# Kernel tuning notes

Measured on AMD Instinct MI355X. Metric: run time of the kernel, lower is better.

## Reference

```python
import jax, jax.numpy as jnp
import numpy as np

B, T, V, H, L = 32, 128, 50257, 1024, 2


def setup_inputs() -> dict:
    key = jax.random.key(0)
    ks = jax.random.split(key, 8)
    s_in = 0.02   # small init to keep gates unsaturated
    return {
        "tokens": jax.random.randint(ks[0], (B, T), 0, V, dtype=jnp.int32),
        "embedding": jax.random.normal(ks[1], (V, H), jnp.float32) * s_in,
        "W_ih": jax.random.normal(ks[2], (L, 4 * H, H), jnp.float32) * s_in,
        "W_hh": jax.random.normal(ks[3], (L, 4 * H, H), jnp.float32) * s_in,
        "b_ih": jax.random.normal(ks[4], (L, 4 * H), jnp.float32) * s_in,
        "b_hh": jax.random.normal(ks[5], (L, 4 * H), jnp.float32) * s_in,
        "W_out": jax.random.normal(ks[6], (V, H), jnp.float32) * s_in,
        "b_out": jax.random.normal(ks[7], (V,), jnp.float32) * s_in,
        "h0": jnp.zeros((L, B, H), jnp.float32),
        "c0": jnp.zeros((L, B, H), jnp.float32),
    }


def reference(tokens, embedding, W_ih, W_hh, b_ih, b_hh, W_out, b_out, h0, c0):
    # Teacher-forced LSTM LM: embed -> L-layer LSTM (PyTorch gate order i,f,g,o)
    # -> vocab projection -> log-softmax. Dropout is identity (p=0 / eval).
    x = embedding[tokens]                      # [B,T,H]
    xs = jnp.swapaxes(x, 0, 1)                 # [T,B,H] time-major for scan
    n_layers = W_ih.shape[0]

    def step(carry, x_t):
        h, c = carry                           # each [L,B,H]
        inp = x_t
        hs, cs = [], []
        for l in range(n_layers):
            gates = inp @ W_ih[l].T + b_ih[l] + h[l] @ W_hh[l].T + b_hh[l]  # [B,4H]
            i_g, f_g, g_g, o_g = jnp.split(gates, 4, axis=-1)
            i_g = jax.nn.sigmoid(i_g)
            f_g = jax.nn.sigmoid(f_g)
            g_g = jnp.tanh(g_g)
            o_g = jax.nn.sigmoid(o_g)
            c_new = f_g * c[l] + i_g * g_g
            h_new = o_g * jnp.tanh(c_new)
            hs.append(h_new)
            cs.append(c_new)
            inp = h_new
        return (jnp.stack(hs), jnp.stack(cs)), inp

    (hT, cT), outs = jax.lax.scan(step, (h0, c0), xs)   # outs: [T,B,H]
    outs = jnp.swapaxes(outs, 0, 1)                     # [B,T,H]
    logits = outs @ W_out.T + b_out                     # [B,T,V]
    logp = jax.nn.log_softmax(logits, axis=-1)
    return logp, hT, cT
```

## Files before the change

### kernel.cpp

```cpp
#include <hip/hip_runtime.h>
#include <hip/hip_bf16.h>
#include <cstdint>
#include <cstddef>

#define DEVI __device__ __forceinline__

typedef __attribute__((ext_vector_type(8))) short short8;
typedef __attribute__((ext_vector_type(4))) float f32x4;
using u16 = unsigned short;

constexpr int BSZ = 32, TSZ = 128, VSZ = 50257, HSZ = 1024;
constexpr int M4 = BSZ * TSZ;
constexpr int FH = 4 * HSZ;
constexpr long long OUT_LOGP = (long long)M4 * VSZ;
constexpr int NWRK = 192;
constexpr int NBLK = 256;
constexpr int LDSB = 147584;
constexpr int LDBF = 50258;
constexpr int NNT = 393;
constexpr int CVT_PER = 20;
constexpr int CVTILES = 64 * CVT_PER;

DEVI u16 f2bf(float f) {
  unsigned u = __float_as_uint(f);
  unsigned r = (u + 0x7fffu + ((u >> 16) & 1u)) >> 16;
  return (u16)r;
}
DEVI u16 f2bf_hw(float f) {
  __hip_bfloat16 h = __float2bfloat16(f);
  return __builtin_bit_cast(u16, h);
}
DEVI float bf2f(u16 u) { return __uint_as_float(((unsigned)u) << 16); }
DEVI float sigm(float x) { return 1.f / (1.f + __expf(-x)); }
DEVI float tanh_fast(float x) { return 1.f - 2.f / (1.f + __expf(2.f * x)); }

DEVI f32x4 mfma16(short8 a, short8 b, f32x4 c) {
  return __builtin_amdgcn_mfma_f32_16x16x32_bf16(a, b, c, 0, 0, 0);
}

DEVI void gld16(const void* g, void* l) {
  auto gp = (const __attribute__((address_space(1))) unsigned int*)g;
  auto lp = (__attribute__((address_space(3))) unsigned int*)l;
  __builtin_amdgcn_global_load_lds(gp, lp, 16, 0, 0);
}

DEVI void cohld16x16(const u16* base, short8 (&d)[16]) {
  asm volatile(
      "global_load_dwordx4 %0, %16, off sc0 sc1\n\t"
      "global_load_dwordx4 %1, %16, off offset:64 sc0 sc1\n\t"
      "global_load_dwordx4 %2, %16, off offset:128 sc0 sc1\n\t"
      "global_load_dwordx4 %3, %16, off offset:192 sc0 sc1\n\t"
      "global_load_dwordx4 %4, %16, off offset:256 sc0 sc1\n\t"
      "global_load_dwordx4 %5, %16, off offset:320 sc0 sc1\n\t"
      "global_load_dwordx4 %6, %16, off offset:384 sc0 sc1\n\t"
      "global_load_dwordx4 %7, %16, off offset:448 sc0 sc1\n\t"
      "global_load_dwordx4 %8, %16, off offset:512 sc0 sc1\n\t"
      "global_load_dwordx4 %9, %16, off offset:576 sc0 sc1\n\t"
      "global_load_dwordx4 %10, %16, off offset:640 sc0 sc1\n\t"
      "global_load_dwordx4 %11, %16, off offset:704 sc0 sc1\n\t"
      "global_load_dwordx4 %12, %16, off offset:768 sc0 sc1\n\t"
      "global_load_dwordx4 %13, %16, off offset:832 sc0 sc1\n\t"
      "global_load_dwordx4 %14, %16, off offset:896 sc0 sc1\n\t"
      "global_load_dwordx4 %15, %16, off offset:960 sc0 sc1\n\t"
      "s_waitcnt vmcnt(0)"
      : "=&v"(d[0]), "=&v"(d[1]), "=&v"(d[2]), "=&v"(d[3]),
        "=&v"(d[4]), "=&v"(d[5]), "=&v"(d[6]), "=&v"(d[7]),
        "=&v"(d[8]), "=&v"(d[9]), "=&v"(d[10]), "=&v"(d[11]),
        "=&v"(d[12]), "=&v"(d[13]), "=&v"(d[14]), "=&v"(d[15])
      : "v"(base)
      : "memory");
}
DEVI void cohst2_u16(u16* p0, u16 v0, u16* p1, u16 v1) {
  asm volatile(
      "global_store_short %0, %2, off sc0 sc1\n\t"
      "global_store_short %1, %3, off sc0 sc1\n\t"
      "s_waitcnt vmcnt(0)"
      :: "v"(p0), "v"(p1), "v"((unsigned)v0), "v"((unsigned)v1)
      : "memory");
}
DEVI void cohst1_u16(u16* p0, u16 v0) {
  asm volatile(
      "global_store_short %0, %1, off sc0 sc1\n\t"
      "s_waitcnt vmcnt(0)"
      :: "v"(p0), "v"((unsigned)v0)
      : "memory");
}
DEVI void flagst(unsigned* p, unsigned v) {
  __hip_atomic_store(p, v, __ATOMIC_RELAXED, __HIP_MEMORY_SCOPE_AGENT);
}
DEVI unsigned flagld(const unsigned* p) {
  return __hip_atomic_load(p, __ATOMIC_RELAXED, __HIP_MEMORY_SCOPE_AGENT);
}

DEVI void wait64(const unsigned* f, unsigned g, int l) {
  while (!__all((int)(flagld(f + l) >= g))) __builtin_amdgcn_s_sleep(1);
}
DEVI void wait128(const unsigned* f, unsigned g, int l) {
  for (;;) {
    unsigned a = flagld(f + l);
    unsigned b = flagld(f + 64 + l);
    if (__all((int)((a >= g) && (b >= g)))) break;
    __builtin_amdgcn_s_sleep(1);
  }
}

__global__ void prep_all(const float* __restrict__ bih, const float* __restrict__ bhh,
                         float* __restrict__ bias0, float* __restrict__ rowsum,
                         unsigned* __restrict__ bar, const float* __restrict__ h0,
                         u16* __restrict__ H0, u16* __restrict__ h1init) {
  int i = blockIdx.x * 256 + threadIdx.x;
  H0[i] = f2bf(h0[i]);
  h1init[i] = f2bf(h0[BSZ * HSZ + i]);
  if (i < FH) { bias0[i] = bih[i] + bhh[i]; rowsum[i] = 0.f; }
  if (i < 1024) bar[i] = 0u;
}

__global__ void cvt_bf16(const float* __restrict__ src, u16* __restrict__ dst, int n4) {
  int i = blockIdx.x * blockDim.x + threadIdx.x;
  int stride = gridDim.x * blockDim.x;
  for (; i < n4; i += stride) {
    float4 v = ((const float4*)src)[i];
    ushort4 o; o.x = f2bf(v.x); o.y = f2bf(v.y); o.z = f2bf(v.z); o.w = f2bf(v.w);
    ((ushort4*)dst)[i] = o;
  }
}

__global__ __launch_bounds__(256) void embed_kernel(const int* __restrict__ tok,
                                                    const float* __restrict__ emb,
                                                    u16* __restrict__ X) {
  int m = blockIdx.x;
  int t = m >> 5, b = m & 31;
  int token = tok[b * TSZ + t];
  const float4* src = (const float4*)(emb + (size_t)token * HSZ);
  int i = threadIdx.x;
  float4 v = src[i];
  ushort4 o; o.x = f2bf(v.x); o.y = f2bf(v.y); o.z = f2bf(v.z); o.w = f2bf(v.w);
  *(ushort4*)(X + (size_t)m * HSZ + i * 4) = o;
}

template <int EPI, bool BCVT, bool TMAJ>
DEVI void gemm_tile(char* smemg, const u16* __restrict__ A, const void* __restrict__ Bsrc,
                    void* __restrict__ Cout, const float* __restrict__ bias,
                    float* __restrict__ rowsum, int m0, int n0, int N, int K, int ldc) {
  u16* As = (u16*)smemg;
  u16* Bs = (u16*)(smemg + 8192);
  float* epi = (float*)smemg;
  const int tid = threadIdx.x;
  const int l = tid & 63, wid = tid >> 6;
  const int wm = wid >> 1, wn = wid & 1;

  const int srow = tid >> 2, sq = tid & 3;
  const int arow0 = m0 + srow, arow1 = m0 + 64 + srow;
  int brow0 = n0 + srow;      if (brow0 > N - 1) brow0 = N - 1;
  int brow1 = n0 + 64 + srow; if (brow1 > N - 1) brow1 = N - 1;

  const u16* Bbf = (const u16*)Bsrc;
  const float* Bf32 = (const float*)Bsrc;
  u16* AsW = As + (size_t)(tid >> 6) * 512;
  u16* BsW = Bs + (size_t)(tid >> 6) * 512;

  f32x4 acc[4][4];
  f32x4 z = {0.f, 0.f, 0.f, 0.f};
#pragma unroll
  for (int a = 0; a < 4; ++a)
#pragma unroll
    for (int b = 0; b < 4; ++b) acc[a][b] = z;

  for (int k0 = 0; k0 < K; k0 += 32) {
    gld16(A + (size_t)arow0 * K + k0 + sq * 8, AsW);
    gld16(A + (size_t)arow1 * K + k0 + sq * 8, AsW + 2048);
    if (!BCVT) {
      gld16(Bbf + (size_t)brow0 * K + k0 + sq * 8, BsW);
      gld16(Bbf + (size_t)brow1 * K + k0 + sq * 8, BsW + 2048);
    } else {
      const float* s0 = Bf32 + (size_t)brow0 * K + k0 + sq * 8;
      const float* s1 = Bf32 + (size_t)brow1 * K + k0 + sq * 8;
      float4 x0 = *(const float4*)s0, y0 = *(const float4*)(s0 + 4);
      float4 x1 = *(const float4*)s1, y1 = *(const float4*)(s1 + 4);
      short8 v0, v1;
      v0[0]=(short)f2bf(x0.x); v0[1]=(short)f2bf(x0.y); v0[2]=(short)f2bf(x0.z); v0[3]=(short)f2bf(x0.w);
      v0[4]=(short)f2bf(y0.x); v0[5]=(short)f2bf(y0.y); v0[6]=(short)f2bf(y0.z); v0[7]=(short)f2bf(y0.w);
      v1[0]=(short)f2bf(x1.x); v1[1]=(short)f2bf(x1.y); v1[2]=(short)f2bf(x1.z); v1[3]=(short)f2bf(x1.w);
      v1[4]=(short)f2bf(y1.x); v1[5]=(short)f2bf(y1.y); v1[6]=(short)f2bf(y1.z); v1[7]=(short)f2bf(y1.w);
      *(short8*)&Bs[(size_t)tid * 8] = v0;
      *(short8*)&Bs[(size_t)tid * 8 + 2048] = v1;
    }
    __syncthreads();
    short8 af[4], bfr[4];
#pragma unroll
    for (int x = 0; x < 4; ++x) {
      int ar = wm * 64 + x * 16 + (l & 15);
      af[x] = *(const short8*)&As[ar * 32 + ((l >> 4) << 3)];
      int br = wn * 64 + x * 16 + (l & 15);
      bfr[x] = *(const short8*)&Bs[br * 32 + ((l >> 4) << 3)];
    }
#pragma unroll
    for (int mf = 0; mf < 4; ++mf)
#pragma unroll
      for (int nf = 0; nf < 4; ++nf)
        acc[mf][nf] = mfma16(af[mf], bfr[nf], acc[mf][nf]);
    __syncthreads();
  }

  if constexpr (EPI == 2) {
    u16* C = (u16*)Cout;
#pragma unroll
    for (int mf = 0; mf < 4; ++mf) {
      int rbase = m0 + wm * 64 + mf * 16 + ((l >> 4) << 2);
      float bvr[4];
#pragma unroll
      for (int j = 0; j < 4; ++j) bvr[j] = bias[rbase + j];
#pragma unroll
      for (int nf = 0; nf < 4; ++nf) {
        int cg = n0 + wn * 64 + nf * 16 + (l & 15);
#pragma unroll
        for (int j = 0; j < 4; ++j)
          C[(size_t)(rbase + j) * ldc + cg] = f2bf_hw(acc[mf][nf][j] + bvr[j]);
      }
    }
  } else if constexpr (EPI == 3) {
    u16* C = (u16*)Cout;
    float* ep = epi + wid * 1024;
    const int lq4 = l >> 4, l15e = l & 15;
    float bv[4];
#pragma unroll
    for (int nf = 0; nf < 4; ++nf) {
      int cg = n0 + wn * 64 + nf * 16 + l15e;
      bv[nf] = (cg < N) ? bias[cg] : 0.f;
    }
    const int r8 = l >> 3, c8 = l & 7;
    const int colb8 = n0 + wn * 64 + c8 * 8;
#pragma unroll
    for (int mf = 0; mf < 4; ++mf) {
#pragma unroll
      for (int nf = 0; nf < 4; ++nf)
#pragma unroll
        for (int j = 0; j < 4; ++j)
          ep[(lq4 * 4 + j) * 64 + nf * 16 + l15e] = acc[mf][nf][j] + bv[nf];
      asm volatile("s_waitcnt lgkmcnt(0)" ::: "memory");
      __builtin_amdgcn_sched_barrier(0);
#pragma unroll
      for (int pass = 0; pass < 2; ++pass) {
        const int rr = pass * 8 + r8;
        f32x4 v0 = *(const f32x4*)&ep[rr * 64 + c8 * 8];
        f32x4 v1 = *(const f32x4*)&ep[rr * 64 + c8 * 8 + 4];
        const int row = m0 + wm * 64 + mf * 16 + rr;
        const int orow = TMAJ ? ((row & 31) * TSZ + (row >> 5)) : row;
        float e = 0.f;
        if (colb8 + 7 < N) {
          short8 o;
          o[0]=(short)f2bf_hw(v0[0]); o[1]=(short)f2bf_hw(v0[1]);
          o[2]=(short)f2bf_hw(v0[2]); o[3]=(short)f2bf_hw(v0[3]);
          o[4]=(short)f2bf_hw(v1[0]); o[5]=(short)f2bf_hw(v1[1]);
          o[6]=(short)f2bf_hw(v1[2]); o[7]=(short)f2bf_hw(v1[3]);
          *(short8*)&C[(size_t)orow * ldc + colb8] = o;
          e = __expf(v0[0]) + __expf(v0[1]) + __expf(v0[2]) + __expf(v0[3]) +
              __expf(v1[0]) + __expf(v1[1]) + __expf(v1[2]) + __expf(v1[3]);
        } else {
#pragma unroll
          for (int kk = 0; kk < 8; ++kk) {
            float fv = (kk < 4) ? v0[kk] : v1[kk - 4];
            if (colb8 + kk < N) {
              C[(size_t)orow * ldc + colb8 + kk] = f2bf_hw(fv);
              e += __expf(fv);
            }
          }
        }
        e += __shfl_xor(e, 1, 8); e += __shfl_xor(e, 2, 8); e += __shfl_xor(e, 4, 8);
        if (c8 == 0) atomicAdd(&rowsum[orow], e);
      }
      asm volatile("s_waitcnt lgkmcnt(0)" ::: "memory");
      __builtin_amdgcn_sched_barrier(0);
    }
  } else {
    float* C = (float*)Cout;
    float* ep = epi + wid * 1024;
    const int lq4 = l >> 4, l15e = l & 15;
    float bv[4];
#pragma unroll
    for (int nf = 0; nf < 4; ++nf) {
      int cg = n0 + wn * 64 + nf * 16 + l15e;
      bv[nf] = (cg < N) ? bias[cg] : 0.f;
    }
    const int colbase = n0 + wn * 64 + l15e * 4;
#pragma unroll
    for (int mf = 0; mf < 4; ++mf) {
#pragma unroll
      for (int nf = 0; nf < 4; ++nf)
#pragma unroll
        for (int j = 0; j < 4; ++j)
          ep[(lq4 * 4 + j) * 64 + nf * 16 + l15e] = acc[mf][nf][j] + bv[nf];
      asm volatile("s_waitcnt lgkmcnt(0)" ::: "memory");
      __builtin_amdgcn_sched_barrier(0);
#pragma unroll
      for (int pass = 0; pass < 4; ++pass) {
        const int rr = pass * 4 + lq4;
        f32x4 v = *(const f32x4*)&ep[rr * 64 + l15e * 4];
        const int row = m0 + wm * 64 + mf * 16 + rr;
        const int orow = TMAJ ? ((row & 31) * TSZ + (row >> 5)) : row;
        float e = 0.f;
        if (colbase + 3 < N) {
          *(f32x4*)&C[(size_t)orow * ldc + colbase] = v;
          e = __expf(v[0]) + __expf(v[1]) + __expf(v[2]) + __expf(v[3]);
        } else {
#pragma unroll
          for (int kk = 0; kk < 4; ++kk)
            if (colbase + kk < N) {
              C[(size_t)orow * ldc + colbase + kk] = v[kk];
              e += __expf(v[kk]);
            }
        }
        e += __shfl_xor(e, 1, 16); e += __shfl_xor(e, 2, 16);
        e += __shfl_xor(e, 4, 16); e += __shfl_xor(e, 8, 16);
        if (l15e == 0) atomicAdd(&rowsum[orow], e);
      }
      asm volatile("s_waitcnt lgkmcnt(0)" ::: "memory");
      __builtin_amdgcn_sched_barrier(0);
    }
  }
}

template <int EPI, bool BCVT, int MAP, bool TMAJ>
__global__ __launch_bounds__(256) void gemm_bt(const u16* __restrict__ A,
                                               const void* __restrict__ Bsrc,
                                               void* __restrict__ Cout,
                                               const float* __restrict__ bias,
                                               float* __restrict__ rowsum,
                                               int nm, int nn, int N, int K, int ldc,
                                               int wofs) {
  __shared__ char smemg[16384];
  const int id = blockIdx.x;
  int bm, bn;
  if constexpr (MAP == 2) {
    const int gsz = (int)gridDim.x;
    int wg = ((gsz & 7) == 0) ? (id % 8) * (gsz >> 3) + (id >> 3) : id;
    int w = wofs + wg;
    bm = w / nn; bn = w % nn;
  } else {
    const int gsz = nm * nn;
    int wg = ((gsz & 7) == 0) ? (id % 8) * (gsz >> 3) + (id >> 3) : id;
    bm = wg % nm; bn = wg / nm;
  }
  gemm_tile<EPI, BCVT, TMAJ>(smemg, A, Bsrc, Cout, bias, rowsum,
                             bm * 128, bn * 128, N, K, ldc);
}

struct LstmArgs {
  const u16* G0T;
  const float* Wih;
  const float* Whh;
  const float* bih, *bhh, *c0;
  u16* H0;
  u16* H1;
  const u16* h1init;
  float* out_hc;
  unsigned* bar;
  const float* Wout;
  u16* Woutbf;
  u16* Lbf;
  const float* bout;
  float* rowsum;
  int mode;
};

DEVI void stage_row_q(const float* src, char* row, int sw, int q) {
  for (int kk = 0; kk < 256; kk += 8) {
    float4 x = *(const float4*)(src + kk);
    float4 y = *(const float4*)(src + kk + 4);
    short8 v;
    v[0]=(short)f2bf(x.x); v[1]=(short)f2bf(x.y); v[2]=(short)f2bf(x.z); v[3]=(short)f2bf(x.w);
    v[4]=(short)f2bf(y.x); v[5]=(short)f2bf(y.y); v[6]=(short)f2bf(y.z); v[7]=(short)f2bf(y.w);
    const int kbyte = (q * 256 + kk) * 2;
    *(short8*)(row + (kbyte ^ sw)) = v;
  }
}

DEVI short8 ldsB(const char* lds, int r, int kbyte) {
  return *(const short8*)(lds + (size_t)r * 2048 + (kbyte ^ ((r & 7) << 4)));
}

DEVI void part_wr(float* part, int wstride_log2, int wv, int R, int lq, f32x4 v) {
  *(f32x4*)&part[(wv << wstride_log2) + (R << 4) + ((lq ^ (R & 3)) << 2)] = v;
}
DEVI float part_rd(const float* part, int wstride_log2, int wv, int R, int c) {
  return part[(wv << wstride_log2) + (R << 4) + ((((c >> 2) ^ (R & 3)) << 2)) + (c & 3)];
}

__global__ __launch_bounds__(256, 1) void lstm_coop(LstmArgs A) {
  extern __shared__ char smem[];
  const int wg = blockIdx.x, tid = threadIdx.x;
  const int wv = tid >> 6, l = tid & 63;
  const int l15 = l & 15, lq = l >> 4;
  const int bh = wv >> 1, kh = wv & 1;

  if (wg < 64) {
    char* WL = smem;
    float* part = (float*)(smem + 131072);
    const int j0 = wg << 4;
    {
      const int R = tid >> 2, q = tid & 3;
      const int grow = ((R >> 4) << 10) + j0 + (R & 15);
      stage_row_q(A.Whh + (size_t)grow * HSZ + q * 256, WL + (size_t)R * 2048,
                  (R & 7) << 4, q);
    }
    const int uu = tid & 15, bb = tid >> 4;
    float cst[2];
    cst[0] = A.c0[(size_t)bb * HSZ + j0 + uu];
    cst[1] = A.c0[(size_t)(bb + 16) * HSZ + j0 + uu];
    __syncthreads();
    unsigned* myflag = A.bar + wg;

    for (int t = 0; t < TSZ; ++t) {
      float g0v[4][2];
      {
        const int col = t * 32;
#pragma unroll
        for (int g4 = 0; g4 < 4; ++g4) {
          const u16* gp = A.G0T + (size_t)((g4 << 10) + j0 + uu) * M4 + col;
          g0v[g4][0] = bf2f(gp[bb]);
          g0v[g4][1] = bf2f(gp[bb + 16]);
        }
      }
      if (t > 0) wait64(A.bar, (unsigned)t, l);
      const u16* hprev = A.H0 + (size_t)t * (BSZ * HSZ);
      const u16* hb = hprev + (size_t)(bh * 16 + l15) * HSZ + (kh << 9) + (lq << 3);
      short8 a[16];
      cohld16x16(hb, a);
      __builtin_amdgcn_sched_barrier(0);
      f32x4 acc[4];
      { f32x4 z = {0.f,0.f,0.f,0.f}; acc[0]=z; acc[1]=z; acc[2]=z; acc[3]=z; }
#pragma unroll
      for (int k = 0; k < 16; ++k) {
        const int kbyte = (((kh << 4) + k) << 6) + (lq << 4);
#pragma unroll
        for (int tr = 0; tr < 4; ++tr)
          acc[tr] = mfma16(a[k], ldsB(WL, (tr << 4) + l15, kbyte), acc[tr]);
      }
#pragma unroll
      for (int tr = 0; tr < 4; ++tr)
        part_wr(part, 10, wv, (tr << 4) + l15, lq, acc[tr]);
      __syncthreads();
      const bool last = (t == TSZ - 1);
      u16* hnext = A.H0 + (size_t)(t + 1) * (BSZ * HSZ);
      u16 hv[2];
#pragma unroll
      for (int pp = 0; pp < 2; ++pp) {
        const int b = bb + (pp << 4);
        float gi = g0v[0][pp], gf = g0v[1][pp], gg = g0v[2][pp], go = g0v[3][pp];
#pragma unroll
        for (int kh2 = 0; kh2 < 2; ++kh2) {
          const int w2 = (pp << 1) | kh2;
          gi += part_rd(part, 10, w2, uu, bb);
          gf += part_rd(part, 10, w2, 16 + uu, bb);
          gg += part_rd(part, 10, w2, 32 + uu, bb);
          go += part_rd(part, 10, w2, 48 + uu, bb);
        }
        float i_ = sigm(gi), f_ = sigm(gf), g_ = tanh_fast(gg), o_ = sigm(go);
        float c_ = f_ * cst[pp] + i_ * g_;
        cst[pp] = c_;
        float h_ = o_ * tanh_fast(c_);
        hv[pp] = f2bf(h_);
        if (last) {
          A.out_hc[(size_t)b * HSZ + j0 + uu] = h_;
          A.out_hc[2 * BSZ * HSZ + (size_t)b * HSZ + j0 + uu] = c_;
        }
      }
      cohst2_u16(hnext + (size_t)bb * HSZ + j0 + uu, hv[0],
                 hnext + (size_t)(bb + 16) * HSZ + j0 + uu, hv[1]);
      __syncthreads();
      if (tid == 0) flagst(myflag, (unsigned)(t + 1));
    }
  } else if (wg < NWRK) {
    char* WxL = smem;
    char* WhL = smem + 65536;
    float* part = (float*)(smem + 131072);
    float* biasL = (float*)(smem + 139264);
    const int lw = wg - 64;
    const int j1 = lw << 3;
    {
      const int rr = tid >> 2, q = tid & 3;
      const int r = rr & 31;
      const int grow = FH + ((r >> 3) << 10) + j1 + (r & 7);
      const float* base = (rr >= 32) ? A.Whh : A.Wih;
      char* dst = ((rr >= 32) ? WhL : WxL) + (size_t)r * 2048;
      stage_row_q(base + (size_t)grow * HSZ + q * 256, dst, (r & 7) << 4, q);
    }
    if (tid < 32) {
      const int grow = FH + ((tid >> 3) << 10) + j1 + (tid & 7);
      biasL[tid] = A.bih[grow] + A.bhh[grow];
    }
    const int uu = tid & 7, b1 = tid >> 3;
    float cst = A.c0[BSZ * HSZ + (size_t)b1 * HSZ + j1 + uu];
    __syncthreads();
    unsigned* myflag = A.bar + 64 + lw;

    for (int t = 0; t < TSZ; ++t) {
      wait64(A.bar, (unsigned)(t + 1), l);
      const u16* x1 = A.H0 + (size_t)(t + 1) * (BSZ * HSZ);
      const u16* xb = x1 + (size_t)(bh * 16 + l15) * HSZ + (kh << 9) + (lq << 3);
      short8 ax[16];
      cohld16x16(xb, ax);
      __builtin_amdgcn_sched_barrier(0);
      f32x4 acc[2];
      { f32x4 z = {0.f,0.f,0.f,0.f}; acc[0]=z; acc[1]=z; }
#pragma unroll
      for (int k = 0; k < 16; ++k) {
        const int kbyte = (((kh << 4) + k) << 6) + (lq << 4);
        acc[0] = mfma16(ax[k], ldsB(WxL, l15, kbyte), acc[0]);
        acc[1] = mfma16(ax[k], ldsB(WxL, 16 + l15, kbyte), acc[1]);
      }
      if (t > 0) wait128(A.bar + 64, (unsigned)t, l);
      const u16* hp = (t == 0) ? A.h1init : A.H1 + (size_t)(t - 1) * (BSZ * HSZ);
      const u16* hbp = hp + (size_t)(bh * 16 + l15) * HSZ + (kh << 9) + (lq << 3);
      short8 ah[16];
      cohld16x16(hbp, ah);
      __builtin_amdgcn_sched_barrier(0);
#pragma unroll
      for (int k = 0; k < 16; ++k) {
        const int kbyte = (((kh << 4) + k) << 6) + (lq << 4);
        acc[0] = mfma16(ah[k], ldsB(WhL, l15, kbyte), acc[0]);
        acc[1] = mfma16(ah[k], ldsB(WhL, 16 + l15, kbyte), acc[1]);
      }
#pragma unroll
      for (int tr = 0; tr < 2; ++tr)
        part_wr(part, 9, wv, (tr << 4) + l15, lq, acc[tr]);
      __syncthreads();
      const bool last = (t == TSZ - 1);
      {
        const int c = b1 & 15, ph = b1 >> 4;
        float gi = biasL[uu], gf = biasL[8 + uu], gg = biasL[16 + uu], go = biasL[24 + uu];
#pragma unroll
        for (int kh2 = 0; kh2 < 2; ++kh2) {
          const int w2 = (ph << 1) | kh2;
          gi += part_rd(part, 9, w2, uu, c);
          gf += part_rd(part, 9, w2, 8 + uu, c);
          gg += part_rd(part, 9, w2, 16 + uu, c);
          go += part_rd(part, 9, w2, 24 + uu, c);
        }
        float i_ = sigm(gi), f_ = sigm(gf), g_ = tanh_fast(gg), o_ = sigm(go);
        float c_ = f_ * cst + i_ * g_;
        cst = c_;
        float h_ = o_ * tanh_fast(c_);
        cohst1_u16(A.H1 + (size_t)t * (BSZ * HSZ) + (size_t)b1 * HSZ + j1 + uu, f2bf(h_));
        if (last) {
          A.out_hc[BSZ * HSZ + (size_t)b1 * HSZ + j1 + uu] = h_;
          A.out_hc[3 * BSZ * HSZ + (size_t)b1 * HSZ + j1 + uu] = c_;
        }
      }
      __syncthreads();
      if (tid == 0) flagst(myflag, (unsigned)(t + 1));
    }
  } else {
    const int cid = wg - NWRK;
    if (A.mode >= 1) {
      const int n4 = (int)((size_t)VSZ * HSZ / 4);
      const float4* src = (const float4*)A.Wout;
      ushort4* dst = (ushort4*)A.Woutbf;
      for (int i = cid * 256 + tid; i < n4; i += 64 * 256) {
        float4 v = src[i];
        ushort4 o;
        o.x = f2bf_hw(v.x); o.y = f2bf_hw(v.y); o.z = f2bf_hw(v.z); o.w = f2bf_hw(v.w);
        dst[i] = o;
      }
      asm volatile("s_waitcnt vmcnt(0)" ::: "memory");
      __builtin_amdgcn_fence(__ATOMIC_RELEASE, "agent");
      __syncthreads();
      if (tid == 0) flagst(A.bar + 192 + cid, 1u);
      if (A.mode == 2) {
        wait64(A.bar + 192, 1u, l);
        __syncthreads();
        for (int k = 0; k < CVT_PER; ++k) {
          const int w = cid + (k << 6);
          const int bm = w / NNT, bn = w % NNT;
          wait128(A.bar + 64, (unsigned)(4 * bm + 4), l);
          __syncthreads();
          gemm_tile<3, false, true>(smem, A.H1, A.Woutbf, A.Lbf, A.bout, A.rowsum,
                                    bm * 128, bn * 128, VSZ, HSZ, LDBF);
        }
      }
    }
  }
}

__global__ void lse_kernel(float* __restrict__ rowsum, int n) {
  int i = blockIdx.x * 256 + threadIdx.x;
  if (i < n) rowsum[i] = logf(rowsum[i]);
}

__global__ __launch_bounds__(256) void lsm_finish(float* __restrict__ C,
                                                  const float* __restrict__ lse, int Vd) {
  int row = blockIdx.y;
  size_t start = (size_t)row * (size_t)Vd;
  float s = lse[row];
  int i = blockIdx.x * 256 + threadIdx.x;
  int col = i * 4;
  if (col + 3 < Vd) {
    f32x4* p = (f32x4*)(C + start + col);
    f32x4 v = *p;
    v[0] -= s; v[1] -= s; v[2] -= s; v[3] -= s;
    *p = v;
  } else {
    for (int j = col; j < Vd; ++j) C[start + j] -= s;
  }
}

__global__ __launch_bounds__(256) void lsm_finish_bf(const u16* __restrict__ L,
                                                     float* __restrict__ out,
                                                     const float* __restrict__ rowsum,
                                                     int Vd, int ldl) {
  int row = blockIdx.y;
  float s = logf(rowsum[row]);
  int col = blockIdx.x * 2048 + threadIdx.x * 8;
  const u16* lp = L + (size_t)row * ldl;
  float* op = out + (size_t)row * Vd;
  if (col + 7 < Vd) {
    short8 v = *(const short8*)(lp + col);
    f32x4 a, b;
    a[0] = bf2f((u16)v[0]) - s; a[1] = bf2f((u16)v[1]) - s;
    a[2] = bf2f((u16)v[2]) - s; a[3] = bf2f((u16)v[3]) - s;
    b[0] = bf2f((u16)v[4]) - s; b[1] = bf2f((u16)v[5]) - s;
    b[2] = bf2f((u16)v[6]) - s; b[3] = bf2f((u16)v[7]) - s;
    *(f32x4*)(op + col) = a;
    *(f32x4*)(op + col + 4) = b;
  } else {
    for (int j = col; j < Vd; ++j) op[j] = bf2f(lp[j]) - s;
  }
}

extern "C" void kernel_launch(void* const* d_in, const int* in_sizes, int n_in,
                              void* d_out, int out_size, void* d_ws, size_t ws_size,
                              hipStream_t stream) {
  const int* tokens = (const int*)d_in[0];
  const float* emb = (const float*)d_in[1];
  const float* Wih = (const float*)d_in[2];
  const float* Whh = (const float*)d_in[3];
  const float* bih = (const float*)d_in[4];
  const float* bhh = (const float*)d_in[5];
  const float* Wout = (const float*)d_in[6];
  const float* bout = (const float*)d_in[7];
  const float* h0 = (const float*)d_in[8];
  const float* c0 = (const float*)d_in[9];
  float* out = (float*)d_out;

  char* w = (char*)d_ws;
  size_t o = 0;
  u16* Xbf = (u16*)(w + o);    o += (size_t)M4 * HSZ * 2;
  u16* Wih0bf = (u16*)(w + o); o += (size_t)FH * HSZ * 2;
  u16* G0T = (u16*)(w + o);    o += (size_t)FH * M4 * 2;
  u16* H0 = (u16*)(w + o);     o += (size_t)(TSZ + 1) * BSZ * HSZ * 2;
  u16* H1 = (u16*)(w + o);     o += (size_t)BSZ * TSZ * HSZ * 2;
  u16* h1init = (u16*)(w + o); o += (size_t)BSZ * HSZ * 2;
  float* bias0 = (float*)(w + o);  o += FH * 4;
  float* rowsum = (float*)(w + o); o += M4 * 4;
  unsigned* bar = (unsigned*)(w + o); o += 4096;
  u16* Woutbf = (u16*)(w + o);
  size_t need_full = o + (size_t)VSZ * HSZ * 2;
  u16* Lbf = (u16*)(w + need_full);
  size_t need_lbf = need_full + (size_t)M4 * LDBF * 2;
  const bool bcvt = (ws_size < need_full);
  const bool bf16c = (ws_size >= need_lbf);
  const int mode = bcvt ? 0 : (bf16c ? 2 : 1);

  prep_all<<<128, 256, 0, stream>>>(bih, bhh, bias0, rowsum, bar, h0, H0, h1init);
  cvt_bf16<<<2048, 256, 0, stream>>>(Wih, Wih0bf, FH * HSZ / 4);
  embed_kernel<<<M4, 256, 0, stream>>>(tokens, emb, Xbf);
  gemm_bt<2, false, 0, false><<<32 * 32, 256, 0, stream>>>(
      Wih0bf, Xbf, G0T, bias0, nullptr, 32, 32, M4, HSZ, M4, 0);

  LstmArgs la{G0T, Wih, Whh, bih, bhh, c0, H0, H1, h1init,
              out + (size_t)OUT_LOGP, bar, Wout, Woutbf, Lbf, bout, rowsum, mode};
  void* kargs[] = {&la};
  hipFuncSetAttribute((const void*)lstm_coop, hipFuncAttributeMaxDynamicSharedMemorySize, LDSB);
  hipLaunchCooperativeKernel((const void*)lstm_coop, dim3(NBLK), dim3(256), kargs, LDSB, stream);

  const int TOT = 32 * NNT;
  if (bf16c) {
    gemm_bt<3, false, 2, true><<<TOT - CVTILES, 256, 0, stream>>>(
        H1, Woutbf, Lbf, bout, rowsum, 32, NNT, VSZ, HSZ, LDBF, CVTILES);
    lsm_finish_bf<<<dim3(25, M4), 256, 0, stream>>>(Lbf, out, rowsum, VSZ, LDBF);
  } else if (!bcvt) {
    gemm_bt<1, false, 2, true><<<TOT, 256, 0, stream>>>(
        H1, Woutbf, out, bout, rowsum, 32, NNT, VSZ, HSZ, VSZ, 0);
    lse_kernel<<<16, 256, 0, stream>>>(rowsum, M4);
    lsm_finish<<<dim3((VSZ + 1023) / 1024, M4), 256, 0, stream>>>(out, rowsum, VSZ);
  } else {
    gemm_bt<1, true, 2, true><<<TOT, 256, 0, stream>>>(
        H1, Wout, out, bout, rowsum, 32, NNT, VSZ, HSZ, VSZ, 0);
    lse_kernel<<<16, 256, 0, stream>>>(rowsum, M4);
    lsm_finish<<<dim3((VSZ + 1023) / 1024, M4), 256, 0, stream>>>(out, rowsum, VSZ);
  }
}
```

Baseline: 1.764 ms.

## Double GEMM K-step to 64 with XOR-swizzled LDS layout

Raises the GEMM tile's K-step from 32 to 64 and doubles LDS to 32 KB. This halves the number of barrier pairs per tile and issues two MFMA sub-steps per load phase. Tiles use 128-byte rows with an XOR swizzle to avoid LDS bank conflicts on fragment reads. The conversion-tile count per batch is also reduced. The extra LDS may lower occupancy, and the swizzled gld16 direct-to-LDS writes must match the read pattern.

New measurement: 1.663 ms (median of 2 runs). 1.06x faster.

```diff
diff --git a/kernel.cpp b/kernel.cpp
--- a/kernel.cpp
+++ b/kernel.cpp
@@ -18,7 +18,7 @@
 constexpr int LDSB = 147584;
 constexpr int LDBF = 50258;
 constexpr int NNT = 393;
-constexpr int CVT_PER = 20;
+constexpr int CVT_PER = 12;
 constexpr int CVTILES = 64 * CVT_PER;
 
 DEVI u16 f2bf(float f) {
@@ -143,21 +143,19 @@
                     void* __restrict__ Cout, const float* __restrict__ bias,
                     float* __restrict__ rowsum, int m0, int n0, int N, int K, int ldc) {
   u16* As = (u16*)smemg;
-  u16* Bs = (u16*)(smemg + 8192);
+  u16* Bs = (u16*)(smemg + 16384);
   float* epi = (float*)smemg;
   const int tid = threadIdx.x;
   const int l = tid & 63, wid = tid >> 6;
   const int wm = wid >> 1, wn = wid & 1;
 
-  const int srow = tid >> 2, sq = tid & 3;
-  const int arow0 = m0 + srow, arow1 = m0 + 64 + srow;
-  int brow0 = n0 + srow;      if (brow0 > N - 1) brow0 = N - 1;
-  int brow1 = n0 + 64 + srow; if (brow1 > N - 1) brow1 = N - 1;
+  const int srow8 = tid >> 3;
+  const int scol = ((tid & 7) * 8) ^ ((srow8 & 7) << 3);
+  u16* AsW = As + (size_t)(tid >> 6) * 8 * 64;
+  u16* BsW = Bs + (size_t)(tid >> 6) * 8 * 64;
 
   const u16* Bbf = (const u16*)Bsrc;
   const float* Bf32 = (const float*)Bsrc;
-  u16* AsW = As + (size_t)(tid >> 6) * 512;
-  u16* BsW = Bs + (size_t)(tid >> 6) * 512;
 
   f32x4 acc[4][4];
   f32x4 z = {0.f, 0.f, 0.f, 0.f};
@@ -166,39 +164,53 @@
 #pragma unroll
     for (int b = 0; b < 4; ++b) acc[a][b] = z;
 
-  for (int k0 = 0; k0 < K; k0 += 32) {
-    gld16(A + (size_t)arow0 * K + k0 + sq * 8, AsW);
-    gld16(A + (size_t)arow1 * K + k0 + sq * 8, AsW + 2048);
-    if (!BCVT) {
-      gld16(Bbf + (size_t)brow0 * K + k0 + sq * 8, BsW);
-      gld16(Bbf + (size_t)brow1 * K + k0 + sq * 8, BsW + 2048);
-    } else {
-      const float* s0 = Bf32 + (size_t)brow0 * K + k0 + sq * 8;
-      const float* s1 = Bf32 + (size_t)brow1 * K + k0 + sq * 8;
-      float4 x0 = *(const float4*)s0, y0 = *(const float4*)(s0 + 4);
-      float4 x1 = *(const float4*)s1, y1 = *(const float4*)(s1 + 4);
-      short8 v0, v1;
-      v0[0]=(short)f2bf(x0.x); v0[1]=(short)f2bf(x0.y); v0[2]=(short)f2bf(x0.z); v0[3]=(short)f2bf(x0.w);
-      v0[4]=(short)f2bf(y0.x); v0[5]=(short)f2bf(y0.y); v0[6]=(short)f2bf(y0.z); v0[7]=(short)f2bf(y0.w);
-      v1[0]=(short)f2bf(x1.x); v1[1]=(short)f2bf(x1.y); v1[2]=(short)f2bf(x1.z); v1[3]=(short)f2bf(x1.w);
-      v1[4]=(short)f2bf(y1.x); v1[5]=(short)f2bf(y1.y); v1[6]=(short)f2bf(y1.z); v1[7]=(short)f2bf(y1.w);
-      *(short8*)&Bs[(size_t)tid * 8] = v0;
-      *(short8*)&Bs[(size_t)tid * 8 + 2048] = v1;
+  for (int k0 = 0; k0 < K; k0 += 64) {
+#pragma unroll
+    for (int rr = 0; rr < 4; ++rr) {
+      gld16(A + (size_t)(m0 + rr * 32 + srow8) * K + k0 + scol, AsW + rr * 2048);
+      if (!BCVT) {
+        int br = n0 + rr * 32 + srow8; if (br > N - 1) br = N - 1;
+        gld16(Bbf + (size_t)br * K + k0 + scol, BsW + rr * 2048);
+      }
+    }
+    if (BCVT) {
+#pragma unroll
+      for (int half = 0; half < 2; ++half) {
+        const int row = half * 64 + (tid >> 2);
+        int br = n0 + row; if (br > N - 1) br = N - 1;
+        const int c0 = (tid & 3) * 16;
+        const float* s = Bf32 + (size_t)br * K + k0 + c0;
+        const int sw = (row & 7) << 3;
+        float4 x0 = *(const float4*)s,       y0 = *(const float4*)(s + 4);
+        float4 x1 = *(const float4*)(s + 8), y1 = *(const float4*)(s + 12);
+        short8 v0, v1;
+        v0[0]=(short)f2bf(x0.x); v0[1]=(short)f2bf(x0.y); v0[2]=(short)f2bf(x0.z); v0[3]=(short)f2bf(x0.w);
+        v0[4]=(short)f2bf(y0.x); v0[5]=(short)f2bf(y0.y); v0[6]=(short)f2bf(y0.z); v0[7]=(short)f2bf(y0.w);
+        v1[0]=(short)f2bf(x1.x); v1[1]=(short)f2bf(x1.y); v1[2]=(short)f2bf(x1.z); v1[3]=(short)f2bf(x1.w);
+        v1[4]=(short)f2bf(y1.x); v1[5]=(short)f2bf(y1.y); v1[6]=(short)f2bf(y1.z); v1[7]=(short)f2bf(y1.w);
+        *(short8*)&Bs[row * 64 + (c0 ^ sw)] = v0;
+        *(short8*)&Bs[row * 64 + ((c0 + 8) ^ sw)] = v1;
+      }
     }
     __syncthreads();
-    short8 af[4], bfr[4];
-#pragma unroll
-    for (int x = 0; x < 4; ++x) {
-      int ar = wm * 64 + x * 16 + (l & 15);
-      af[x] = *(const short8*)&As[ar * 32 + ((l >> 4) << 3)];
-      int br = wn * 64 + x * 16 + (l & 15);
-      bfr[x] = *(const short8*)&Bs[br * 32 + ((l >> 4) << 3)];
-    }
-#pragma unroll
-    for (int mf = 0; mf < 4; ++mf)
-#pragma unroll
-      for (int nf = 0; nf < 4; ++nf)
-        acc[mf][nf] = mfma16(af[mf], bfr[nf], acc[mf][nf]);
+#pragma unroll
+    for (int ks = 0; ks < 2; ++ks) {
+      short8 af[4], bfr[4];
+#pragma unroll
+      for (int x = 0; x < 4; ++x) {
+        const int ar = wm * 64 + x * 16 + (l & 15);
+        const int ka = (ks * 64 + (l >> 4) * 16) ^ ((ar & 7) << 4);
+        af[x] = *(const short8*)((const char*)As + ar * 128 + ka);
+        const int br = wn * 64 + x * 16 + (l & 15);
+        const int kb = (ks * 64 + (l >> 4) * 16) ^ ((br & 7) << 4);
+        bfr[x] = *(const short8*)((const char*)Bs + br * 128 + kb);
+      }
+#pragma unroll
+      for (int mf = 0; mf < 4; ++mf)
+#pragma unroll
+        for (int nf = 0; nf < 4; ++nf)
+          acc[mf][nf] = mfma16(af[mf], bfr[nf], acc[mf][nf]);
+    }
     __syncthreads();
   }
 
@@ -328,7 +340,7 @@
                                                float* __restrict__ rowsum,
                                                int nm, int nn, int N, int K, int ldc,
                                                int wofs) {
-  __shared__ char smemg[16384];
+  __shared__ char smemg[32768];
   const int id = blockIdx.x;
   int bm, bn;
   if constexpr (MAP == 2) {
```
